# Kernel tuning notes

Hardware: AMD Instinct MI355X
Metric: run time of the kernel (lower is better)

## Reference

```python
import jax, jax.numpy as jnp
import numpy as np

N_ATOMS = 8192
N_EDGES = 262144
N_MOL = 128
F = 128
R = 20
CUTOFF = 5.0
L = 3
EPS = 1e-8


def setup_inputs() -> dict:
    key = jax.random.key(0)
    ks = jax.random.split(key, 20)
    sc = 0.05  # weight init scale for numerical stability
    inp = {
        "z": jax.random.randint(ks[0], (N_ATOMS,), 0, 100, dtype=jnp.int32),
        "pos": jax.random.uniform(ks[1], (N_ATOMS, 3), dtype=jnp.float32),
        "edge_src": jax.random.randint(ks[2], (N_EDGES,), 0, N_ATOMS, dtype=jnp.int32),
        "edge_dst": jax.random.randint(ks[3], (N_EDGES,), 0, N_ATOMS, dtype=jnp.int32),
        "mol_idx": jnp.sort(jax.random.randint(ks[4], (N_ATOMS,), 0, N_MOL, dtype=jnp.int32)),
        "embed": jax.random.normal(ks[5], (100, F), dtype=jnp.float32) * sc,
        "msg_w1": jax.random.normal(ks[6], (L, F, F), dtype=jnp.float32) * sc,
        "msg_b1": jnp.zeros((L, F), jnp.float32),
        "msg_w2": jax.random.normal(ks[7], (L, F, 3 * F), dtype=jnp.float32) * sc,
        "msg_b2": jnp.zeros((L, 3 * F), jnp.float32),
        "rbf_w": jax.random.normal(ks[8], (L, R, 3 * F), dtype=jnp.float32) * sc,
        "rbf_b": jnp.zeros((L, 3 * F), jnp.float32),
        "upd_u": jax.random.normal(ks[9], (L, F, F), dtype=jnp.float32) * sc,
        "upd_v": jax.random.normal(ks[10], (L, F, F), dtype=jnp.float32) * sc,
        "upd_a1": jax.random.normal(ks[11], (L, 2 * F, F), dtype=jnp.float32) * sc,
        "upd_a1b": jnp.zeros((L, F), jnp.float32),
        "upd_a2": jax.random.normal(ks[12], (L, F, 3 * F), dtype=jnp.float32) * sc,
        "upd_a2b": jnp.zeros((L, 3 * F), jnp.float32),
        "out_w1": jax.random.normal(ks[13], (F, F), dtype=jnp.float32) * sc,
        "out_b1": jnp.zeros((F,), jnp.float32),
        "out_w2": jax.random.normal(ks[14], (F, 1), dtype=jnp.float32) * sc,
        "out_b2": jnp.zeros((1,), jnp.float32),
    }
    return inp


def _painn_forward(z, pos, edge_src, edge_dst, mol_idx, embed,
                   msg_w1, msg_b1, msg_w2, msg_b2, rbf_w, rbf_b,
                   upd_u, upd_v, upd_a1, upd_a1b, upd_a2, upd_a2b,
                   out_w1, out_b1, out_w2, out_b2):
    n = z.shape[0]
    s = embed[z]                                  # [N,F]
    v = jnp.zeros((n, 3, F), s.dtype)             # [N,3,F]

    rij = pos[edge_dst] - pos[edge_src]           # [E,3]
    d = jnp.sqrt(jnp.sum(rij * rij, axis=-1) + EPS)  # [E]
    unit = rij / d[:, None]                       # [E,3]
    freq = jnp.arange(1, R + 1, dtype=s.dtype) * (jnp.pi / CUTOFF)
    rbf = jnp.sin(d[:, None] * freq[None, :]) / d[:, None]          # [E,R]
    fc = 0.5 * (jnp.cos(jnp.pi * d / CUTOFF) + 1.0) * (d < CUTOFF)  # [E]

    for l in range(L):
        # --- message block ---
        phi = jax.nn.silu(s @ msg_w1[l] + msg_b1[l]) @ msg_w2[l] + msg_b2[l]  # [N,3F]
        wfilt = (rbf @ rbf_w[l] + rbf_b[l]) * fc[:, None]                      # [E,3F]
        m = phi[edge_src] * wfilt                                              # [E,3F]
        ds_e, dvv, dvs = m[:, :F], m[:, F:2 * F], m[:, 2 * F:]
        ds = jax.ops.segment_sum(ds_e, edge_dst, num_segments=n)
        dv_e = v[edge_src] * dvv[:, None, :] + unit[:, :, None] * dvs[:, None, :]  # [E,3,F]
        dv = jax.ops.segment_sum(dv_e, edge_dst, num_segments=n)
        s = s + ds
        v = v + dv
        # --- update block ---
        uv = jnp.einsum('ncf,fg->ncg', v, upd_u[l])   # [N,3,F]
        vv = jnp.einsum('ncf,fg->ncg', v, upd_v[l])   # [N,3,F]
        vv_norm = jnp.sqrt(jnp.sum(vv * vv, axis=1) + EPS)  # [N,F]
        a = jax.nn.silu(jnp.concatenate([s, vv_norm], axis=-1) @ upd_a1[l] + upd_a1b[l])
        a = a @ upd_a2[l] + upd_a2b[l]                # [N,3F]
        a_vv, a_sv, a_ss = a[:, :F], a[:, F:2 * F], a[:, 2 * F:]
        s = s + a_ss + a_sv * jnp.sum(uv * vv, axis=1)
        v = v + a_vv[:, None, :] * uv

    atom_out = jax.nn.silu(s @ out_w1 + out_b1) @ out_w2 + out_b2  # [N,1]
    return jax.ops.segment_sum(atom_out, mol_idx, num_segments=N_MOL)  # [M,1]


def reference(z, pos, edge_src, edge_dst, mol_idx, embed,
              msg_w1, msg_b1, msg_w2, msg_b2, rbf_w, rbf_b,
              upd_u, upd_v, upd_a1, upd_a1b, upd_a2, upd_a2b,
              out_w1, out_b1, out_w2, out_b2):
    return _painn_forward(z, pos, edge_src, edge_dst, mol_idx, embed,
                          msg_w1, msg_b1, msg_w2, msg_b2, rbf_w, rbf_b,
                          upd_u, upd_v, upd_a1, upd_a1b, upd_a2, upd_a2b,
                          out_w1, out_b1, out_w2, out_b2)
```

## Files before the change

kernel.cpp:

```cpp
#include <hip/hip_runtime.h>
#include <hip/hip_bf16.h>
#include <math.h>

#define N_ATOMS 8192
#define N_EDGES 262144
#define N_MOL   128
#define FDIM    128
#define RDIM    20
#define LLAYERS 3
#define CUTOFF  5.0f
#define EPSV    1e-8f
#define PI_F    3.14159265358979323846f

typedef __attribute__((ext_vector_type(8))) short bf16x8;
typedef __attribute__((ext_vector_type(4))) float f32x4;

#define VPLANE 1048576

__device__ __forceinline__ ushort f2bf(float x) {
    uint b = __float_as_uint(x);
    return (ushort)((b + 0x7fffu + ((b >> 16) & 1u)) >> 16);
}

__global__ void k_wconv(const float* __restrict__ w1, const float* __restrict__ w2,
                        const float* __restrict__ uu, const float* __restrict__ uvw,
                        const float* __restrict__ a1, const float* __restrict__ a2,
                        const float* __restrict__ ow1, ushort* __restrict__ WT) {
    int i = blockIdx.x * 256 + threadIdx.x;
    float v;
    if (i < 49152) {
        int idx = i; int l = idx >> 14; idx &= 16383;
        int n = idx >> 7, k = idx & 127;
        v = w1[l*16384 + k*128 + n];
    } else if (i < 196608) {
        int idx = i - 49152; int l = idx / 49152; idx -= l * 49152;
        int n = idx >> 7, k = idx & 127;
        v = w2[l*49152 + k*384 + n];
    } else if (i < 294912) {
        int idx = i - 196608; int l = idx >> 15; idx &= 32767;
        int n = idx >> 7, k = idx & 127;
        v = (n < 128) ? uu[l*16384 + k*128 + n] : uvw[l*16384 + k*128 + (n-128)];
    } else if (i < 393216) {
        int idx = i - 294912; int l = idx >> 15; idx &= 32767;
        int n = idx >> 8, k = idx & 255;
        v = a1[l*32768 + k*128 + n];
    } else if (i < 540672) {
        int idx = i - 393216; int l = idx / 49152; idx -= l * 49152;
        int n = idx >> 7, k = idx & 127;
        v = a2[l*49152 + k*384 + n];
    } else {
        int idx = i - 540672;
        int n = idx >> 7, k = idx & 127;
        v = ow1[k*128 + n];
    }
    WT[i] = f2bf(v);
}

__global__ void k_embed(const int* __restrict__ z, const float* __restrict__ embed,
                        float* __restrict__ S, ushort* __restrict__ SBF) {
    int i = blockIdx.x * 256 + threadIdx.x;
    int a = i >> 7, k = i & 127;
    float v = embed[(size_t)z[a] * FDIM + k];
    S[i] = v; SBF[i] = f2bf(v);
}

__global__ void k_hist(const int* __restrict__ edst, int* __restrict__ CNT) {
    int e = blockIdx.x * 256 + threadIdx.x;
    if (e < N_EDGES) atomicAdd(&CNT[edst[e]], 1);
}

__global__ __launch_bounds__(1024) void k_scan(const int* __restrict__ CNT,
                                               int* __restrict__ OFF, int* __restrict__ CUR) {
    __shared__ int part[1024];
    int t = threadIdx.x;
    int loc[8];
    int run = 0;
    #pragma unroll
    for (int i = 0; i < 8; i++) { int c = CNT[t*8 + i]; loc[i] = run; run += c; }
    part[t] = run;
    __syncthreads();
    for (int off = 1; off < 1024; off <<= 1) {
        int v = 0;
        if (t >= off) v = part[t - off];
        __syncthreads();
        part[t] += v;
        __syncthreads();
    }
    int ebase = (t > 0) ? part[t-1] : 0;
    #pragma unroll
    for (int i = 0; i < 8; i++) { int o = ebase + loc[i]; OFF[t*8+i] = o; CUR[t*8+i] = o; }
    if (t == 1023) OFF[8192] = part[1023];
}

__global__ void k_edges(const float* __restrict__ pos, const int* __restrict__ esrc,
                        const int* __restrict__ edst, int* __restrict__ CUR,
                        float* __restrict__ RBF, float* __restrict__ UNITFC,
                        int* __restrict__ SRCS) {
    int e = blockIdx.x * 256 + threadIdx.x;
    if (e >= N_EDGES) return;
    int s = esrc[e], d = edst[e];
    int p = atomicAdd(&CUR[d], 1);
    float rx = pos[d*3+0] - pos[s*3+0];
    float ry = pos[d*3+1] - pos[s*3+1];
    float rz = pos[d*3+2] - pos[s*3+2];
    float dd = sqrtf(rx*rx + ry*ry + rz*rz + EPSV);
    float inv = 1.0f / dd;
    float fc = (dd < CUTOFF) ? 0.5f * (cosf(dd * (PI_F / CUTOFF)) + 1.0f) : 0.0f;
    float4 u4; u4.x = rx*inv; u4.y = ry*inv; u4.z = rz*inv; u4.w = fc;
    *(float4*)&UNITFC[(size_t)p*4] = u4;
    SRCS[p] = s;
    float rb[RDIM];
    #pragma unroll
    for (int r = 0; r < RDIM; r++) {
        float freq = (float)(r + 1) * (PI_F / CUTOFF);
        rb[r] = sinf(dd * freq) * inv;
    }
    float4* out = (float4*)&RBF[(size_t)p * RDIM];
    #pragma unroll
    for (int q = 0; q < 5; q++) {
        float4 o; o.x = rb[q*4]; o.y = rb[q*4+1]; o.z = rb[q*4+2]; o.w = rb[q*4+3];
        out[q] = o;
    }
}

__global__ __launch_bounds__(256) void k_msg(
    const ushort* __restrict__ SBF, const ushort* __restrict__ W1T, const float* __restrict__ b1,
    const ushort* __restrict__ W2T, const float* __restrict__ b2, ushort* __restrict__ PHIB)
{
    int tid = threadIdx.x;
    int w = tid >> 6, l = tid & 63;
    int bm = blockIdx.x * 16;
    int lrow = l & 15, lk = (l >> 4) * 8;
    __shared__ ushort Hs[16][136];

    f32x4 acc[2] = {{0.f,0.f,0.f,0.f},{0.f,0.f,0.f,0.f}};
    #pragma unroll
    for (int k0 = 0; k0 < 128; k0 += 32) {
        bf16x8 af = *(const bf16x8*)&SBF[(size_t)(bm + lrow)*128 + k0 + lk];
        #pragma unroll
        for (int t = 0; t < 2; t++) {
            int n = (2*w + t)*16 + lrow;
            bf16x8 bf = *(const bf16x8*)&W1T[(size_t)n*128 + k0 + lk];
            acc[t] = __builtin_amdgcn_mfma_f32_16x16x32_bf16(af, bf, acc[t], 0, 0, 0);
        }
    }
    #pragma unroll
    for (int t = 0; t < 2; t++) {
        int col = (2*w + t)*16 + lrow;
        float bv = b1[col];
        #pragma unroll
        for (int j = 0; j < 4; j++) {
            int row = (l >> 4)*4 + j;
            float val = acc[t][j] + bv;
            val = val / (1.0f + __expf(-val));
            Hs[row][col] = f2bf(val);
        }
    }
    __syncthreads();

    f32x4 acc2[6];
    #pragma unroll
    for (int t = 0; t < 6; t++) acc2[t] = (f32x4){0.f,0.f,0.f,0.f};
    #pragma unroll
    for (int k0 = 0; k0 < 128; k0 += 32) {
        bf16x8 af = *(const bf16x8*)&Hs[lrow][k0 + lk];
        #pragma unroll
        for (int t = 0; t < 6; t++) {
            int n = (6*w + t)*16 + lrow;
            bf16x8 bf = *(const bf16x8*)&W2T[(size_t)n*128 + k0 + lk];
            acc2[t] = __builtin_amdgcn_mfma_f32_16x16x32_bf16(af, bf, acc2[t], 0, 0, 0);
        }
    }
    #pragma unroll
    for (int t = 0; t < 6; t++) {
        int col = (6*w + t)*16 + lrow;
        float bv = b2[col];
        #pragma unroll
        for (int j = 0; j < 4; j++) {
            int row = bm + (l >> 4)*4 + j;
            PHIB[(size_t)row*384 + col] = f2bf(acc2[t][j] + bv);
        }
    }
}

__global__ __launch_bounds__(192) void k_aggregate(
    const ushort* __restrict__ PHIB, const ushort* __restrict__ VBFA,
    float* __restrict__ S, ushort* __restrict__ SBF,
    float* __restrict__ V, ushort* __restrict__ VBFB,
    const float* __restrict__ RBF, const float* __restrict__ UNITFC,
    const int* __restrict__ SRCS, const int* __restrict__ OFF,
    const float* __restrict__ rbfw, const float* __restrict__ rbfb)
{
    int a = blockIdx.x;
    int tid = threadIdx.x;
    int g = tid >> 6;
    int c0 = 2 * (tid & 63);

    float2 w[RDIM];
    const float* wc = rbfw + g*128 + c0;
    #pragma unroll
    for (int r = 0; r < RDIM; r++) { w[r].x = wc[r*384]; w[r].y = wc[r*384 + 1]; }
    float2 bb; bb.x = rbfb[g*128 + c0]; bb.y = rbfb[g*128 + c0 + 1];

    __shared__ int sSrc[64];
    __shared__ float4 sRBF[320];
    __shared__ float4 sUFC[64];
    __shared__ float avs[3][128];

    int beg = OFF[a], end = OFF[a + 1];
    float2 d; d.x = 0.f; d.y = 0.f;
    float2 A0, A1, A2v;
    A0.x=A0.y=A1.x=A1.y=A2v.x=A2v.y=0.f;

    for (int p0 = beg; p0 < end; p0 += 64) {
        int n = end - p0; if (n > 64) n = 64;
        __syncthreads();
        if (tid < n) sSrc[tid] = SRCS[p0 + tid];
        for (int i = tid; i < n; i += 192)
            sUFC[i] = *(const float4*)(UNITFC + (size_t)(p0 + i) * 4);
        {
            const float4* rsrc = (const float4*)(RBF + (size_t)p0 * RDIM);
            for (int i = tid; i < n*5; i += 192) sRBF[i] = rsrc[i];
        }
        __syncthreads();

        uint phA[4], u0A[4], u1A[4], u2A[4];
        uint phB[4], u0B[4], u1B[4], u2B[4];
        uint phC[4], u0C[4], u1C[4], u2C[4];

        auto grpLoad = [&](int base, uint* ph, uint* u0, uint* u1, uint* u2) {
            #pragma unroll
            for (int j = 0; j < 4; j++) {
                int q = base + j;
                int src = sSrc[(q < n) ? q : 0];
                size_t pb = (size_t)src * 128;
                ph[j] = *(const uint*)&PHIB[(size_t)src*384 + g*128 + c0];
                if (g == 1) {
                    u0[j] = *(const uint*)&VBFA[pb + c0];
                    u1[j] = *(const uint*)&VBFA[pb + VPLANE + c0];
                    u2[j] = *(const uint*)&VBFA[pb + 2*VPLANE + c0];
                }
            }
        };
        auto grpComp = [&](int base, uint* ph, uint* u0, uint* u1, uint* u2) {
            #pragma unroll
            for (int j = 0; j < 4; j++) {
                int q = base + j;
                if (q >= n) break;
                float4 r0 = sRBF[q*5+0], r1 = sRBF[q*5+1], r2 = sRBF[q*5+2],
                       r3 = sRBF[q*5+3], r4 = sRBF[q*5+4];
                float4 ufc = sUFC[q];
                float2 f = bb;
                f.x += r0.x*w[0].x;   f.y += r0.x*w[0].y;
                f.x += r0.y*w[1].x;   f.y += r0.y*w[1].y;
                f.x += r0.z*w[2].x;   f.y += r0.z*w[2].y;
                f.x += r0.w*w[3].x;   f.y += r0.w*w[3].y;
                f.x += r1.x*w[4].x;   f.y += r1.x*w[4].y;
                f.x += r1.y*w[5].x;   f.y += r1.y*w[5].y;
                f.x += r1.z*w[6].x;   f.y += r1.z*w[6].y;
                f.x += r1.w*w[7].x;   f.y += r1.w*w[7].y;
                f.x += r2.x*w[8].x;   f.y += r2.x*w[8].y;
                f.x += r2.y*w[9].x;   f.y += r2.y*w[9].y;
                f.x += r2.z*w[10].x;  f.y += r2.z*w[10].y;
                f.x += r2.w*w[11].x;  f.y += r2.w*w[11].y;
                f.x += r3.x*w[12].x;  f.y += r3.x*w[12].y;
                f.x += r3.y*w[13].x;  f.y += r3.y*w[13].y;
                f.x += r3.z*w[14].x;  f.y += r3.z*w[14].y;
                f.x += r3.w*w[15].x;  f.y += r3.w*w[15].y;
                f.x += r4.x*w[16].x;  f.y += r4.x*w[16].y;
                f.x += r4.y*w[17].x;  f.y += r4.y*w[17].y;
                f.x += r4.z*w[18].x;  f.y += r4.z*w[18].y;
                f.x += r4.w*w[19].x;  f.y += r4.w*w[19].y;
                uint up = ph[j];
                float m0 = __uint_as_float(up << 16)         * (f.x * ufc.w);
                float m1 = __uint_as_float(up & 0xffff0000u) * (f.y * ufc.w);
                if (g == 0) {
                    d.x += m0; d.y += m1;
                } else if (g == 1) {
                    A0.x  += __uint_as_float(u0[j] << 16)         * m0;
                    A0.y  += __uint_as_float(u0[j] & 0xffff0000u) * m1;
                    A1.x  += __uint_as_float(u1[j] << 16)         * m0;
                    A1.y  += __uint_as_float(u1[j] & 0xffff0000u) * m1;
                    A2v.x += __uint_as_float(u2[j] << 16)         * m0;
                    A2v.y += __uint_as_float(u2[j] & 0xffff0000u) * m1;
                } else {
                    A0.x  += ufc.x * m0; A0.y  += ufc.x * m1;
                    A1.x  += ufc.y * m0; A1.y  += ufc.y * m1;
                    A2v.x += ufc.z * m0; A2v.y += ufc.z * m1;
                }
            }
        };

        grpLoad(0, phA, u0A, u1A, u2A);
        grpLoad(4, phB, u0B, u1B, u2B);
        grpLoad(8, phC, u0C, u1C, u2C);
        for (int q0 = 0; q0 < n; q0 += 12) {
            grpComp(q0,      phA, u0A, u1A, u2A);
            grpLoad(q0 + 12, phA, u0A, u1A, u2A);
            grpComp(q0 + 4,  phB, u0B, u1B, u2B);
            grpLoad(q0 + 16, phB, u0B, u1B, u2B);
            grpComp(q0 + 8,  phC, u0C, u1C, u2C);
            grpLoad(q0 + 20, phC, u0C, u1C, u2C);
        }
    }

    if (g == 1) {
        avs[0][c0] = A0.x;  avs[0][c0+1] = A0.y;
        avs[1][c0] = A1.x;  avs[1][c0+1] = A1.y;
        avs[2][c0] = A2v.x; avs[2][c0+1] = A2v.y;
    }
    __syncthreads();
    if (g == 0) {
        size_t sb = (size_t)a*128 + c0;
        float2 s2 = *(float2*)&S[sb];
        s2.x += d.x; s2.y += d.y;
        *(float2*)&S[sb] = s2;
        SBF[sb] = f2bf(s2.x); SBF[sb+1] = f2bf(s2.y);
    } else if (g == 2) {
        float own0[3] = {A0.x, A1.x, A2v.x};
        float own1[3] = {A0.y, A1.y, A2v.y};
        #pragma unroll
        for (int c = 0; c < 3; c++) {
            size_t vb = (size_t)c*VPLANE + (size_t)a*128 + c0;
            float2 vi = *(const float2*)&V[vb];
            vi.x += avs[c][c0]     + own0[c];
            vi.y += avs[c][c0 + 1] + own1[c];
            *(float2*)&V[vb] = vi;
            VBFB[vb] = f2bf(vi.x); VBFB[vb+1] = f2bf(vi.y);
        }
    }
}

__global__ __launch_bounds__(256) void k_upd(
    const ushort* __restrict__ VBFB, const ushort* __restrict__ UVT,
    const ushort* __restrict__ SBF_in,
    const ushort* __restrict__ A1T, const float* __restrict__ a1b,
    const ushort* __restrict__ A2T, const float* __restrict__ a2b,
    float* __restrict__ S, ushort* __restrict__ SBF,
    float* __restrict__ V, ushort* __restrict__ VBFA)
{
    int tid = threadIdx.x;
    int w = tid >> 6, l = tid & 63;
    int bm = blockIdx.x * 16;
    int lrow = l & 15, lk = (l >> 4) * 8;
    __shared__ ushort sVVN[16][136];
    __shared__ ushort Hs[16][136];

    f32x4 au[3][2], av[3][2];
    #pragma unroll
    for (int c = 0; c < 3; c++)
        #pragma unroll
        for (int t = 0; t < 2; t++) {
            au[c][t] = (f32x4){0.f,0.f,0.f,0.f};
            av[c][t] = (f32x4){0.f,0.f,0.f,0.f};
        }
    #pragma unroll
    for (int k0 = 0; k0 < 128; k0 += 32) {
        bf16x8 af[3];
        #pragma unroll
        for (int c = 0; c < 3; c++)
            af[c] = *(const bf16x8*)&VBFB[(size_t)c*VPLANE + (size_t)(bm + lrow)*128 + k0 + lk];
        #pragma unroll
        for (int t = 0; t < 2; t++) {
            int nu = (2*w + t)*16 + lrow;
            bf16x8 bu = *(const bf16x8*)&UVT[(size_t)nu*128 + k0 + lk];
            bf16x8 bv = *(const bf16x8*)&UVT[(size_t)(nu + 128)*128 + k0 + lk];
            #pragma unroll
            for (int c = 0; c < 3; c++) {
                au[c][t] = __builtin_amdgcn_mfma_f32_16x16x32_bf16(af[c], bu, au[c][t], 0, 0, 0);
                av[c][t] = __builtin_amdgcn_mfma_f32_16x16x32_bf16(af[c], bv, av[c][t], 0, 0, 0);
            }
        }
    }
    float dotr[2][4], uvr[3][2][4];
    #pragma unroll
    for (int t = 0; t < 2; t++) {
        int k = (2*w + t)*16 + lrow;
        #pragma unroll
        for (int j = 0; j < 4; j++) {
            int row = (l >> 4)*4 + j;
            float u0 = au[0][t][j], u1 = au[1][t][j], u2 = au[2][t][j];
            float v0 = av[0][t][j], v1 = av[1][t][j], v2 = av[2][t][j];
            uvr[0][t][j] = u0; uvr[1][t][j] = u1; uvr[2][t][j] = u2;
            dotr[t][j] = u0*v0 + u1*v1 + u2*v2;
            sVVN[row][k] = f2bf(sqrtf(v0*v0 + v1*v1 + v2*v2 + EPSV));
        }
    }
    __syncthreads();

    f32x4 acc[2] = {{0.f,0.f,0.f,0.f},{0.f,0.f,0.f,0.f}};
    #pragma unroll
    for (int k0 = 0; k0 < 256; k0 += 32) {
        bf16x8 af;
        if (k0 < 128) af = *(const bf16x8*)&SBF_in[(size_t)(bm + lrow)*128 + k0 + lk];
        else          af = *(const bf16x8*)&sVVN[lrow][k0 + lk - 128];
        #pragma unroll
        for (int t = 0; t < 2; t++) {
            int n = (2*w + t)*16 + lrow;
            bf16x8 bf = *(const bf16x8*)&A1T[(size_t)n*256 + k0 + lk];
            acc[t] = __builtin_amdgcn_mfma_f32_16x16x32_bf16(af, bf, acc[t], 0, 0, 0);
        }
    }
    #pragma unroll
    for (int t = 0; t < 2; t++) {
        int col = (2*w + t)*16 + lrow;
        float bv = a1b[col];
        #pragma unroll
        for (int j = 0; j < 4; j++) {
            int row = (l >> 4)*4 + j;
            float val = acc[t][j] + bv;
            val = val / (1.0f + __expf(-val));
            Hs[row][col] = f2bf(val);
        }
    }
    __syncthreads();

    f32x4 c_vv[2], c_sv[2], c_ss[2];
    #pragma unroll
    for (int t = 0; t < 2; t++) {
        c_vv[t] = (f32x4){0.f,0.f,0.f,0.f};
        c_sv[t] = (f32x4){0.f,0.f,0.f,0.f};
        c_ss[t] = (f32x4){0.f,0.f,0.f,0.f};
    }
    #pragma unroll
    for (int k0 = 0; k0 < 128; k0 += 32) {
        bf16x8 af = *(const bf16x8*)&Hs[lrow][k0 + lk];
        #pragma unroll
        for (int t = 0; t < 2; t++) {
            int n0 = (2*w + t)*16 + lrow;
            bf16x8 b0 = *(const bf16x8*)&A2T[(size_t)n0*128 + k0 + lk];
            bf16x8 b1 = *(const bf16x8*)&A2T[(size_t)(n0 + 128)*128 + k0 + lk];
            bf16x8 b2 = *(const bf16x8*)&A2T[(size_t)(n0 + 256)*128 + k0 + lk];
            c_vv[t] = __builtin_amdgcn_mfma_f32_16x16x32_bf16(af, b0, c_vv[t], 0, 0, 0);
            c_sv[t] = __builtin_amdgcn_mfma_f32_16x16x32_bf16(af, b1, c_sv[t], 0, 0, 0);
            c_ss[t] = __builtin_amdgcn_mfma_f32_16x16x32_bf16(af, b2, c_ss[t], 0, 0, 0);
        }
    }
    #pragma unroll
    for (int t = 0; t < 2; t++) {
        int k = (2*w + t)*16 + lrow;
        float b_vv = a2b[k], b_sv = a2b[128 + k], b_ss = a2b[256 + k];
        #pragma unroll
        for (int j = 0; j < 4; j++) {
            int a = bm + (l >> 4)*4 + j;
            size_t base = (size_t)a*128 + k;
            float vv = c_vv[t][j] + b_vv;
            float sv = c_sv[t][j] + b_sv;
            float ss = c_ss[t][j] + b_ss;
            float sn = S[base] + ss + sv * dotr[t][j];
            S[base] = sn; SBF[base] = f2bf(sn);
            #pragma unroll
            for (int c = 0; c < 3; c++) {
                size_t vb = (size_t)c*VPLANE + base;
                float nv = V[vb] + vv * uvr[c][t][j];
                V[vb] = nv; VBFA[vb] = f2bf(nv);
            }
        }
    }
}

__global__ __launch_bounds__(64) void k_readout(
    const ushort* __restrict__ SBF, const ushort* __restrict__ OW1T,
    const float* __restrict__ b1, const float* __restrict__ w2,
    const float* __restrict__ b2v, const int* __restrict__ mol,
    float* __restrict__ out)
{
    int l = threadIdx.x;
    int bm = blockIdx.x * 16;
    int lrow = l & 15, lk = (l >> 4) * 8;
    __shared__ float Hs[16][132];

    f32x4 acc[8];
    #pragma unroll
    for (int t = 0; t < 8; t++) acc[t] = (f32x4){0.f,0.f,0.f,0.f};
    #pragma unroll
    for (int k0 = 0; k0 < 128; k0 += 32) {
        bf16x8 af = *(const bf16x8*)&SBF[(size_t)(bm + lrow)*128 + k0 + lk];
        #pragma unroll
        for (int t = 0; t < 8; t++) {
            bf16x8 bf = *(const bf16x8*)&OW1T[(size_t)(t*16 + lrow)*128 + k0 + lk];
            acc[t] = __builtin_amdgcn_mfma_f32_16x16x32_bf16(af, bf, acc[t], 0, 0, 0);
        }
    }
    #pragma unroll
    for (int t = 0; t < 8; t++) {
        int col = t*16 + lrow;
        float bv = b1[col];
        #pragma unroll
        for (int j = 0; j < 4; j++) {
            int row = (l >> 4)*4 + j;
            float val = acc[t][j] + bv;
            Hs[row][col] = val / (1.0f + __expf(-val));
        }
    }
    __syncthreads();
    if (l < 16) {
        float s = b2v[0];
        #pragma unroll 8
        for (int k = 0; k < 128; k++) s += Hs[l][k] * w2[k];
        atomicAdd(&out[mol[bm + l]], s);
    }
}

extern "C" void kernel_launch(void* const* d_in, const int* in_sizes, int n_in,
                              void* d_out, int out_size, void* d_ws, size_t ws_size,
                              hipStream_t stream) {
    const int*   z      = (const int*)d_in[0];
    const float* pos    = (const float*)d_in[1];
    const int*   esrc   = (const int*)d_in[2];
    const int*   edst   = (const int*)d_in[3];
    const int*   mol    = (const int*)d_in[4];
    const float* embed  = (const float*)d_in[5];
    const float* msg_w1 = (const float*)d_in[6];
    const float* msg_b1 = (const float*)d_in[7];
    const float* msg_w2 = (const float*)d_in[8];
    const float* msg_b2 = (const float*)d_in[9];
    const float* rbf_w  = (const float*)d_in[10];
    const float* rbf_b  = (const float*)d_in[11];
    const float* upd_u  = (const float*)d_in[12];
    const float* upd_v  = (const float*)d_in[13];
    const float* upd_a1 = (const float*)d_in[14];
    const float* upd_a1b= (const float*)d_in[15];
    const float* upd_a2 = (const float*)d_in[16];
    const float* upd_a2b= (const float*)d_in[17];
    const float* out_w1 = (const float*)d_in[18];
    const float* out_b1 = (const float*)d_in[19];
    const float* out_w2 = (const float*)d_in[20];
    const float* out_b2 = (const float*)d_in[21];

    float* ws = (float*)d_ws;
    float* S      = ws; ws += 1048576;
    float* V      = ws; ws += 3145728;
    float* RBF    = ws; ws += 5242880;
    float* UNITFC = ws; ws += 1048576;
    ushort* PHIB  = (ushort*)ws; ws += 1572864;
    ushort* VBFA  = (ushort*)ws; ws += 1572864;
    ushort* VBFB  = (ushort*)ws; ws += 1572864;
    ushort* SBF   = (ushort*)ws; ws += 524288;
    ushort* WT    = (ushort*)ws; ws += 278528;
    int* CNT  = (int*)ws;
    int* OFF  = CNT + 8192;
    int* CUR  = OFF + 8193;
    int* SRCS = CUR + 8192;

    hipMemsetAsync(V, 0, 3145728 * sizeof(float), stream);
    hipMemsetAsync(VBFA, 0, 3145728 * sizeof(ushort), stream);
    hipMemsetAsync(CNT, 0, 8192 * sizeof(int), stream);
    hipMemsetAsync(d_out, 0, N_MOL * sizeof(float), stream);

    k_wconv<<<2176, 256, 0, stream>>>(msg_w1, msg_w2, upd_u, upd_v, upd_a1, upd_a2, out_w1, WT);
    k_embed<<<4096, 256, 0, stream>>>(z, embed, S, SBF);
    k_hist<<<1024, 256, 0, stream>>>(edst, CNT);
    k_scan<<<1, 1024, 0, stream>>>(CNT, OFF, CUR);
    k_edges<<<1024, 256, 0, stream>>>(pos, esrc, edst, CUR, RBF, UNITFC, SRCS);

    for (int l = 0; l < LLAYERS; l++) {
        const ushort* W1T = WT + l*16384;
        const ushort* W2T = WT + 49152  + l*49152;
        const ushort* UVT = WT + 196608 + l*32768;
        const ushort* A1T = WT + 294912 + l*32768;
        const ushort* A2T = WT + 393216 + l*49152;

        k_msg<<<512, 256, 0, stream>>>(SBF, W1T, msg_b1 + (size_t)l*128,
                                       W2T, msg_b2 + (size_t)l*384, PHIB);
        k_aggregate<<<8192, 192, 0, stream>>>(PHIB, VBFA, S, SBF, V, VBFB, RBF, UNITFC,
            SRCS, OFF, rbf_w + (size_t)l*20*384, rbf_b + (size_t)l*384);
        k_upd<<<512, 256, 0, stream>>>(VBFB, UVT, SBF, A1T, upd_a1b + (size_t)l*128,
            A2T, upd_a2b + (size_t)l*384, S, SBF, V, VBFA);
    }

    k_readout<<<512, 64, 0, stream>>>(SBF, WT + 540672, out_b1, out_w2, out_b2,
                                      mol, (float*)d_out);
}
```

Measured before the change: 704.3 us.

## Specialize first-layer aggregation for zero vectors and process four atoms per block

Templates the aggregation kernel on a first-layer flag. At layer zero the vector features are zero, so the VBFA gather and group-1 work are skipped and V is written directly instead of being read, which lets the two large V/VBFA memsets go. Each block now handles four atoms, cutting the grid from 8192 to 2048 blocks and amortizing the per-block RBF weight loads into registers. The gather prefetch is shortened from three staged groups to two-deep double buffering, which lowers register pressure but hides less memory latency.

```diff
diff --git a/kernel.cpp b/kernel.cpp
--- a/kernel.cpp
+++ b/kernel.cpp
@@ -183,6 +183,7 @@
     }
 }
 
+template<bool L0>
 __global__ __launch_bounds__(192) void k_aggregate(
     const ushort* __restrict__ PHIB, const ushort* __restrict__ VBFA,
     float* __restrict__ S, ushort* __restrict__ SBF,
@@ -191,7 +192,6 @@
     const int* __restrict__ SRCS, const int* __restrict__ OFF,
     const float* __restrict__ rbfw, const float* __restrict__ rbfb)
 {
-    int a = blockIdx.x;
     int tid = threadIdx.x;
     int g = tid >> 6;
     int c0 = 2 * (tid & 63);
@@ -207,126 +207,126 @@
     __shared__ float4 sUFC[64];
     __shared__ float avs[3][128];
 
-    int beg = OFF[a], end = OFF[a + 1];
-    float2 d; d.x = 0.f; d.y = 0.f;
-    float2 A0, A1, A2v;
-    A0.x=A0.y=A1.x=A1.y=A2v.x=A2v.y=0.f;
-
-    for (int p0 = beg; p0 < end; p0 += 64) {
-        int n = end - p0; if (n > 64) n = 64;
-        __syncthreads();
-        if (tid < n) sSrc[tid] = SRCS[p0 + tid];
-        for (int i = tid; i < n; i += 192)
-            sUFC[i] = *(const float4*)(UNITFC + (size_t)(p0 + i) * 4);
-        {
-            const float4* rsrc = (const float4*)(RBF + (size_t)p0 * RDIM);
-            for (int i = tid; i < n*5; i += 192) sRBF[i] = rsrc[i];
-        }
-        __syncthreads();
-
-        uint phA[4], u0A[4], u1A[4], u2A[4];
-        uint phB[4], u0B[4], u1B[4], u2B[4];
-        uint phC[4], u0C[4], u1C[4], u2C[4];
-
-        auto grpLoad = [&](int base, uint* ph, uint* u0, uint* u1, uint* u2) {
-            #pragma unroll
-            for (int j = 0; j < 4; j++) {
-                int q = base + j;
-                int src = sSrc[(q < n) ? q : 0];
-                size_t pb = (size_t)src * 128;
-                ph[j] = *(const uint*)&PHIB[(size_t)src*384 + g*128 + c0];
-                if (g == 1) {
-                    u0[j] = *(const uint*)&VBFA[pb + c0];
-                    u1[j] = *(const uint*)&VBFA[pb + VPLANE + c0];
-                    u2[j] = *(const uint*)&VBFA[pb + 2*VPLANE + c0];
+    for (int ai = 0; ai < 4; ai++) {
+        int a = blockIdx.x * 4 + ai;
+        int beg = OFF[a], end = OFF[a + 1];
+        float2 d; d.x = 0.f; d.y = 0.f;
+        float2 A0, A1, A2v;
+        A0.x=A0.y=A1.x=A1.y=A2v.x=A2v.y=0.f;
+
+        for (int p0 = beg; p0 < end; p0 += 64) {
+            int n = end - p0; if (n > 64) n = 64;
+            __syncthreads();
+            if (tid < n) sSrc[tid] = SRCS[p0 + tid];
+            for (int i = tid; i < n; i += 192)
+                sUFC[i] = *(const float4*)(UNITFC + (size_t)(p0 + i) * 4);
+            {
+                const float4* rsrc = (const float4*)(RBF + (size_t)p0 * RDIM);
+                for (int i = tid; i < n*5; i += 192) sRBF[i] = rsrc[i];
+            }
+            __syncthreads();
+
+            if (L0 && g == 1) continue;
+
+            uint phA[4], u0A[4], u1A[4], u2A[4];
+            uint phB[4], u0B[4], u1B[4], u2B[4];
+
+            auto grpLoad = [&](int base, uint* ph, uint* u0, uint* u1, uint* u2) {
+                #pragma unroll
+                for (int j = 0; j < 4; j++) {
+                    int q = base + j;
+                    int src = sSrc[(q < n) ? q : 0];
+                    size_t pb = (size_t)src * 128;
+                    ph[j] = *(const uint*)&PHIB[(size_t)src*384 + g*128 + c0];
+                    if (!L0 && g == 1) {
+                        u0[j] = *(const uint*)&VBFA[pb + c0];
+                        u1[j] = *(const uint*)&VBFA[pb + VPLANE + c0];
+                        u2[j] = *(const uint*)&VBFA[pb + 2*VPLANE + c0];
+                    }
+                }
+            };
+            grpLoad(0, phA, u0A, u1A, u2A);
+            for (int q0 = 0; q0 < n; q0 += 4) {
+                if (q0 + 4 < n) grpLoad(q0 + 4, phB, u0B, u1B, u2B);
+                #pragma unroll
+                for (int j = 0; j < 4; j++) {
+                    int q = q0 + j;
+                    if (q >= n) break;
+                    float4 r0 = sRBF[q*5+0], r1 = sRBF[q*5+1], r2 = sRBF[q*5+2],
+                           r3 = sRBF[q*5+3], r4 = sRBF[q*5+4];
+                    float4 ufc = sUFC[q];
+                    float2 f = bb;
+                    f.x += r0.x*w[0].x;   f.y += r0.x*w[0].y;
+                    f.x += r0.y*w[1].x;   f.y += r0.y*w[1].y;
+                    f.x += r0.z*w[2].x;   f.y += r0.z*w[2].y;
+                    f.x += r0.w*w[3].x;   f.y += r0.w*w[3].y;
+                    f.x += r1.x*w[4].x;   f.y += r1.x*w[4].y;
+                    f.x += r1.y*w[5].x;   f.y += r1.y*w[5].y;
+                    f.x += r1.z*w[6].x;   f.y += r1.z*w[6].y;
+                    f.x += r1.w*w[7].x;   f.y += r1.w*w[7].y;
+                    f.x += r2.x*w[8].x;   f.y += r2.x*w[8].y;
+                    f.x += r2.y*w[9].x;   f.y += r2.y*w[9].y;
+                    f.x += r2.z*w[10].x;  f.y += r2.z*w[10].y;
+                    f.x += r2.w*w[11].x;  f.y += r2.w*w[11].y;
+                    f.x += r3.x*w[12].x;  f.y += r3.x*w[12].y;
+                    f.x += r3.y*w[13].x;  f.y += r3.y*w[13].y;
+                    f.x += r3.z*w[14].x;  f.y += r3.z*w[14].y;
+                    f.x += r3.w*w[15].x;  f.y += r3.w*w[15].y;
+                    f.x += r4.x*w[16].x;  f.y += r4.x*w[16].y;
+                    f.x += r4.y*w[17].x;  f.y += r4.y*w[17].y;
+                    f.x += r4.z*w[18].x;  f.y += r4.z*w[18].y;
+                    f.x += r4.w*w[19].x;  f.y += r4.w*w[19].y;
+                    uint up = phA[j];
+                    float m0 = __uint_as_float(up << 16)         * (f.x * ufc.w);
+                    float m1 = __uint_as_float(up & 0xffff0000u) * (f.y * ufc.w);
+                    if (g == 0) {
+                        d.x += m0; d.y += m1;
+                    } else if (g == 1) {
+                        A0.x  += __uint_as_float(u0A[j] << 16)         * m0;
+                        A0.y  += __uint_as_float(u0A[j] & 0xffff0000u) * m1;
+                        A1.x  += __uint_as_float(u1A[j] << 16)         * m0;
+                        A1.y  += __uint_as_float(u1A[j] & 0xffff0000u) * m1;
+                        A2v.x += __uint_as_float(u2A[j] << 16)         * m0;
+                        A2v.y += __uint_as_float(u2A[j] & 0xffff0000u) * m1;
+                    } else {
+                        A0.x  += ufc.x * m0; A0.y  += ufc.x * m1;
+                        A1.x  += ufc.y * m0; A1.y  += ufc.y * m1;
+                        A2v.x += ufc.z * m0; A2v.y += ufc.z * m1;
+                    }
+                }
+                #pragma unroll
+                for (int j = 0; j < 4; j++) {
+                    phA[j] = phB[j]; u0A[j] = u0B[j]; u1A[j] = u1B[j]; u2A[j] = u2B[j];
                 }
             }
-        };
-        auto grpComp = [&](int base, uint* ph, uint* u0, uint* u1, uint* u2) {
+        }
+
+        if (g == 1) {
+            avs[0][c0] = A0.x;  avs[0][c0+1] = A0.y;
+            avs[1][c0] = A1.x;  avs[1][c0+1] = A1.y;
+            avs[2][c0] = A2v.x; avs[2][c0+1] = A2v.y;
+        }
+        __syncthreads();
+        if (g == 0) {
+            size_t sb = (size_t)a*128 + c0;
+            float2 s2 = *(float2*)&S[sb];
+            s2.x += d.x; s2.y += d.y;
+            *(float2*)&S[sb] = s2;
+            SBF[sb] = f2bf(s2.x); SBF[sb+1] = f2bf(s2.y);
+        } else if (g == 2) {
+            float own0[3] = {A0.x, A1.x, A2v.x};
+            float own1[3] = {A0.y, A1.y, A2v.y};
             #pragma unroll
-            for (int j = 0; j < 4; j++) {
-                int q = base + j;
-                if (q >= n) break;
-                float4 r0 = sRBF[q*5+0], r1 = sRBF[q*5+1], r2 = sRBF[q*5+2],
-                       r3 = sRBF[q*5+3], r4 = sRBF[q*5+4];
-                float4 ufc = sUFC[q];
-                float2 f = bb;
-                f.x += r0.x*w[0].x;   f.y += r0.x*w[0].y;
-                f.x += r0.y*w[1].x;   f.y += r0.y*w[1].y;
-                f.x += r0.z*w[2].x;   f.y += r0.z*w[2].y;
-                f.x += r0.w*w[3].x;   f.y += r0.w*w[3].y;
-                f.x += r1.x*w[4].x;   f.y += r1.x*w[4].y;
-                f.x += r1.y*w[5].x;   f.y += r1.y*w[5].y;
-                f.x += r1.z*w[6].x;   f.y += r1.z*w[6].y;
-                f.x += r1.w*w[7].x;   f.y += r1.w*w[7].y;
-                f.x += r2.x*w[8].x;   f.y += r2.x*w[8].y;
-                f.x += r2.y*w[9].x;   f.y += r2.y*w[9].y;
-                f.x += r2.z*w[10].x;  f.y += r2.z*w[10].y;
-                f.x += r2.w*w[11].x;  f.y += r2.w*w[11].y;
-                f.x += r3.x*w[12].x;  f.y += r3.x*w[12].y;
-                f.x += r3.y*w[13].x;  f.y += r3.y*w[13].y;
-                f.x += r3.z*w[14].x;  f.y += r3.z*w[14].y;
-                f.x += r3.w*w[15].x;  f.y += r3.w*w[15].y;
-                f.x += r4.x*w[16].x;  f.y += r4.x*w[16].y;
-                f.x += r4.y*w[17].x;  f.y += r4.y*w[17].y;
-                f.x += r4.z*w[18].x;  f.y += r4.z*w[18].y;
-                f.x += r4.w*w[19].x;  f.y += r4.w*w[19].y;
-                uint up = ph[j];
-                float m0 = __uint_as_float(up << 16)         * (f.x * ufc.w);
-                float m1 = __uint_as_float(up & 0xffff0000u) * (f.y * ufc.w);
-                if (g == 0) {
-                    d.x += m0; d.y += m1;
-                } else if (g == 1) {
-                    A0.x  += __uint_as_float(u0[j] << 16)         * m0;
-                    A0.y  += __uint_as_float(u0[j] & 0xffff0000u) * m1;
-                    A1.x  += __uint_as_float(u1[j] << 16)         * m0;
-                    A1.y  += __uint_as_float(u1[j] & 0xffff0000u) * m1;
-                    A2v.x += __uint_as_float(u2[j] << 16)         * m0;
-                    A2v.y += __uint_as_float(u2[j] & 0xffff0000u) * m1;
-                } else {
-                    A0.x  += ufc.x * m0; A0.y  += ufc.x * m1;
-                    A1.x  += ufc.y * m0; A1.y  += ufc.y * m1;
-                    A2v.x += ufc.z * m0; A2v.y += ufc.z * m1;
-                }
+            for (int c = 0; c < 3; c++) {
+                size_t vb = (size_t)c*VPLANE + (size_t)a*128 + c0;
+                float2 vi;
+                if (L0) { vi.x = 0.f; vi.y = 0.f; }
+                else    vi = *(const float2*)&V[vb];
+                vi.x += avs[c][c0]     + own0[c];
+                vi.y += avs[c][c0 + 1] + own1[c];
+                *(float2*)&V[vb] = vi;
+                VBFB[vb] = f2bf(vi.x); VBFB[vb+1] = f2bf(vi.y);
             }
-        };
-
-        grpLoad(0, phA, u0A, u1A, u2A);
-        grpLoad(4, phB, u0B, u1B, u2B);
-        grpLoad(8, phC, u0C, u1C, u2C);
-        for (int q0 = 0; q0 < n; q0 += 12) {
-            grpComp(q0,      phA, u0A, u1A, u2A);
-            grpLoad(q0 + 12, phA, u0A, u1A, u2A);
-            grpComp(q0 + 4,  phB, u0B, u1B, u2B);
-            grpLoad(q0 + 16, phB, u0B, u1B, u2B);
-            grpComp(q0 + 8,  phC, u0C, u1C, u2C);
-            grpLoad(q0 + 20, phC, u0C, u1C, u2C);
-        }
-    }
-
-    if (g == 1) {
-        avs[0][c0] = A0.x;  avs[0][c0+1] = A0.y;
-        avs[1][c0] = A1.x;  avs[1][c0+1] = A1.y;
-        avs[2][c0] = A2v.x; avs[2][c0+1] = A2v.y;
-    }
-    __syncthreads();
-    if (g == 0) {
-        size_t sb = (size_t)a*128 + c0;
-        float2 s2 = *(float2*)&S[sb];
-        s2.x += d.x; s2.y += d.y;
-        *(float2*)&S[sb] = s2;
-        SBF[sb] = f2bf(s2.x); SBF[sb+1] = f2bf(s2.y);
-    } else if (g == 2) {
-        float own0[3] = {A0.x, A1.x, A2v.x};
-        float own1[3] = {A0.y, A1.y, A2v.y};
-        #pragma unroll
-        for (int c = 0; c < 3; c++) {
-            size_t vb = (size_t)c*VPLANE + (size_t)a*128 + c0;
-            float2 vi = *(const float2*)&V[vb];
-            vi.x += avs[c][c0]     + own0[c];
-            vi.y += avs[c][c0 + 1] + own1[c];
-            *(float2*)&V[vb] = vi;
-            VBFB[vb] = f2bf(vi.x); VBFB[vb+1] = f2bf(vi.y);
         }
     }
 }
@@ -543,8 +543,6 @@
     int* CUR  = OFF + 8193;
     int* SRCS = CUR + 8192;
 
-    hipMemsetAsync(V, 0, 3145728 * sizeof(float), stream);
-    hipMemsetAsync(VBFA, 0, 3145728 * sizeof(ushort), stream);
     hipMemsetAsync(CNT, 0, 8192 * sizeof(int), stream);
     hipMemsetAsync(d_out, 0, N_MOL * sizeof(float), stream);
 
@@ -563,8 +561,12 @@
 
         k_msg<<<512, 256, 0, stream>>>(SBF, W1T, msg_b1 + (size_t)l*128,
                                        W2T, msg_b2 + (size_t)l*384, PHIB);
-        k_aggregate<<<8192, 192, 0, stream>>>(PHIB, VBFA, S, SBF, V, VBFB, RBF, UNITFC,
-            SRCS, OFF, rbf_w + (size_t)l*20*384, rbf_b + (size_t)l*384);
+        if (l == 0)
+            k_aggregate<true><<<2048, 192, 0, stream>>>(PHIB, VBFA, S, SBF, V, VBFB,
+                RBF, UNITFC, SRCS, OFF, rbf_w + (size_t)l*20*384, rbf_b + (size_t)l*384);
+        else
+            k_aggregate<false><<<2048, 192, 0, stream>>>(PHIB, VBFA, S, SBF, V, VBFB,
+                RBF, UNITFC, SRCS, OFF, rbf_w + (size_t)l*20*384, rbf_b + (size_t)l*384);
         k_upd<<<512, 256, 0, stream>>>(VBFB, UVT, SBF, A1T, upd_a1b + (size_t)l*128,
             A2T, upd_a2b + (size_t)l*384, S, SBF, V, VBFA);
     }
```

New measurement: 654.8 us. 1.08x faster.
